# Performance work log

Hardware: AMD Instinct MI355X
Metric: run time of the kernel (lower is better)

The kernel has to match this reference:

```python
import jax, jax.numpy as jnp
import numpy as np

ALPHA_LINK = 2.0   # init arg alpha_link
TOP_K = 4096       # init arg top_k
BATCH = 65536
NUM_CLASSES = 4096


def setup_inputs() -> dict:
    key = jax.random.key(0)
    k1, k2, k3 = jax.random.split(key, 3)
    y_pred = jax.random.normal(k1, (BATCH, NUM_CLASSES), dtype=jnp.float32)
    y_true = jax.random.randint(k2, (BATCH,), 0, NUM_CLASSES, dtype=jnp.int32)
    # dense boolean link table: link_table[gt, pred] == True iff pred in link[gt]
    link_table = jax.random.randint(k3, (NUM_CLASSES, NUM_CLASSES), 0, 2, dtype=jnp.int32).astype(bool)
    return {"y_pred": y_pred, "y_true": y_true, "link_table": link_table}


def reference(y_pred, y_true, link_table):
    # vectorized replacement of the per-sample dict-lookup loop
    pred = jnp.argmax(y_pred, axis=1)                     # [B]
    linked = link_table[y_true, pred]                     # [B] bool
    # factor = alpha_link iff pred != gt and pred in link[gt]; else 1
    factor = jnp.where((pred != y_true) & linked, ALPHA_LINK, 1.0)
    # cross_entropy(reduction='none'), weight=None
    logp = jax.nn.log_softmax(y_pred, axis=1)             # [B, C]
    ce = -jnp.take_along_axis(logp, y_true[:, None], axis=1)[:, 0]  # [B]
    worst_k, _ = jax.lax.top_k(factor * ce, TOP_K)        # [TOP_K]
    return jnp.mean(worst_k)
```

## Files before the change

kernel.cpp:

```cpp
#include <hip/hip_runtime.h>

#define NCLS   4096
#define BATCHN 65536
#define TOPK   4096
#define ALPHA  2.0f

__global__ void detect_int32_kernel(const unsigned int* __restrict__ lt,
                                    int* __restrict__ flag) {
    int tid = threadIdx.x;
    unsigned int bad = 0;
    for (int i = tid; i < 1024; i += 64) bad |= (lt[i] > 1u) ? 1u : 0u;
    unsigned long long mask = __ballot(bad != 0);
    if (tid == 0) flag[0] = (mask == 0ULL) ? 1 : 0;
}

__device__ inline void amax_comb(float& m, int& mi, float om, int omi) {
    if (om > m || (om == m && omi < mi)) { m = om; mi = omi; }
}

__global__ __launch_bounds__(256) void row_loss_kernel(
    const float* __restrict__ yp, const int* __restrict__ yt,
    const unsigned char* __restrict__ lt, const int* __restrict__ flag,
    float* __restrict__ losses) {
    const int b   = blockIdx.x;
    const int tid = threadIdx.x;
    const float4* row = reinterpret_cast<const float4*>(yp + (size_t)b * NCLS);

    float4 v0 = row[0 * 256 + tid];
    float4 v1 = row[1 * 256 + tid];
    float4 v2 = row[2 * 256 + tid];
    float4 v3 = row[3 * 256 + tid];

    float m = -3.4e38f; int mi = 0;
    {
        const int c0 = tid * 4;
        if (v0.x > m) { m = v0.x; mi = c0 + 0; }
        if (v0.y > m) { m = v0.y; mi = c0 + 1; }
        if (v0.z > m) { m = v0.z; mi = c0 + 2; }
        if (v0.w > m) { m = v0.w; mi = c0 + 3; }
        const int c1 = 1024 + tid * 4;
        if (v1.x > m) { m = v1.x; mi = c1 + 0; }
        if (v1.y > m) { m = v1.y; mi = c1 + 1; }
        if (v1.z > m) { m = v1.z; mi = c1 + 2; }
        if (v1.w > m) { m = v1.w; mi = c1 + 3; }
        const int c2 = 2048 + tid * 4;
        if (v2.x > m) { m = v2.x; mi = c2 + 0; }
        if (v2.y > m) { m = v2.y; mi = c2 + 1; }
        if (v2.z > m) { m = v2.z; mi = c2 + 2; }
        if (v2.w > m) { m = v2.w; mi = c2 + 3; }
        const int c3 = 3072 + tid * 4;
        if (v3.x > m) { m = v3.x; mi = c3 + 0; }
        if (v3.y > m) { m = v3.y; mi = c3 + 1; }
        if (v3.z > m) { m = v3.z; mi = c3 + 2; }
        if (v3.w > m) { m = v3.w; mi = c3 + 3; }
    }

    #pragma unroll
    for (int off = 32; off > 0; off >>= 1) {
        float om  = __shfl_down(m, off, 64);
        int   omi = __shfl_down(mi, off, 64);
        amax_comb(m, mi, om, omi);
    }

    __shared__ float wmax[4];
    __shared__ int   wmi[4];
    __shared__ float wsum[4];
    __shared__ float s_M;
    __shared__ int   s_pred;
    __shared__ float s_true;

    const int wid = tid >> 6, lane = tid & 63;
    if (lane == 0) { wmax[wid] = m; wmi[wid] = mi; }
    __syncthreads();
    if (tid == 0) {
        float M = wmax[0]; int P = wmi[0];
        amax_comb(M, P, wmax[1], wmi[1]);
        amax_comb(M, P, wmax[2], wmi[2]);
        amax_comb(M, P, wmax[3], wmi[3]);
        s_M = M; s_pred = P;
    }
    __syncthreads();
    const float M = s_M;

    float sum = 0.f;
    sum += __expf(v0.x - M); sum += __expf(v0.y - M);
    sum += __expf(v0.z - M); sum += __expf(v0.w - M);
    sum += __expf(v1.x - M); sum += __expf(v1.y - M);
    sum += __expf(v1.z - M); sum += __expf(v1.w - M);
    sum += __expf(v2.x - M); sum += __expf(v2.y - M);
    sum += __expf(v2.z - M); sum += __expf(v2.w - M);
    sum += __expf(v3.x - M); sum += __expf(v3.y - M);
    sum += __expf(v3.z - M); sum += __expf(v3.w - M);

    #pragma unroll
    for (int off = 32; off > 0; off >>= 1) sum += __shfl_down(sum, off, 64);

    const int gt = yt[b];
    if (tid == ((gt >> 2) & 255)) {
        const int j = gt >> 10, k = gt & 3;
        float4 vv = (j == 0) ? v0 : (j == 1) ? v1 : (j == 2) ? v2 : v3;
        float t = (k == 0) ? vv.x : (k == 1) ? vv.y : (k == 2) ? vv.z : vv.w;
        s_true = t;
    }
    if (lane == 0) wsum[wid] = sum;
    __syncthreads();

    if (tid == 0) {
        float tot = wsum[0] + wsum[1] + wsum[2] + wsum[3];
        float ce  = logf(tot) + s_M - s_true;
        int pred  = s_pred;
        float factor = 1.0f;
        if (pred != gt) {
            size_t idx = (size_t)gt * NCLS + (size_t)pred;
            int linked = flag[0] ? ((const int*)lt)[idx] : (int)lt[idx];
            if (linked) factor = ALPHA;
        }
        losses[b] = factor * ce;
    }
}

__device__ void find_thresh_4096(unsigned int* hist, unsigned int* superb,
                                 int* s_t, unsigned int* s_above,
                                 unsigned int kneed, int tid) {
    if (tid < 64) {
        unsigned int s = 0;
        #pragma unroll 8
        for (int i = 0; i < 64; ++i) s += hist[tid * 64 + i];
        superb[tid] = s;
    }
    __syncthreads();
    if (tid == 0) {
        unsigned int cum = 0; int sb = 63;
        for (; sb > 0; --sb) {
            if (cum + superb[sb] >= kneed) break;
            cum += superb[sb];
        }
        const int lo = sb * 64;
        int t = lo + 63;
        for (; t > lo; --t) {
            if (cum + hist[t] >= kneed) break;
            cum += hist[t];
        }
        *s_t = t; *s_above = cum;
    }
    __syncthreads();
}

__global__ __launch_bounds__(1024) void topk_mean_kernel(
    const float* __restrict__ losses, float* __restrict__ out) {
    __shared__ unsigned int hist[4096];
    __shared__ unsigned int superb[64];
    __shared__ int          s_t;
    __shared__ unsigned int s_above;
    __shared__ unsigned int s_cntgt;
    __shared__ double       dsum[1024];

    const int tid = threadIdx.x;
    const int N = BATCHN, K = TOPK;
    unsigned int kneed = K;

    for (int i = tid; i < 4096; i += 1024) hist[i] = 0;
    __syncthreads();
    for (int i = tid; i < N; i += 1024) {
        unsigned int key = __float_as_uint(losses[i]);
        atomicAdd(&hist[key >> 20], 1u);
    }
    __syncthreads();
    find_thresh_4096(hist, superb, &s_t, &s_above, kneed, tid);
    const unsigned int t1 = (unsigned int)s_t;
    kneed -= s_above;
    __syncthreads();

    for (int i = tid; i < 4096; i += 1024) hist[i] = 0;
    __syncthreads();
    for (int i = tid; i < N; i += 1024) {
        unsigned int key = __float_as_uint(losses[i]);
        if ((key >> 20) == t1) atomicAdd(&hist[(key >> 8) & 0xFFFu], 1u);
    }
    __syncthreads();
    find_thresh_4096(hist, superb, &s_t, &s_above, kneed, tid);
    const unsigned int t2 = (unsigned int)s_t;
    kneed -= s_above;
    __syncthreads();

    const unsigned int pref = (t1 << 12) | t2;
    for (int i = tid; i < 256; i += 1024) hist[i] = 0;
    __syncthreads();
    for (int i = tid; i < N; i += 1024) {
        unsigned int key = __float_as_uint(losses[i]);
        if ((key >> 8) == pref) atomicAdd(&hist[key & 0xFFu], 1u);
    }
    __syncthreads();
    if (tid == 0) {
        unsigned int cum = 0; int t = 255;
        for (; t > 0; --t) {
            if (cum + hist[t] >= kneed) break;
            cum += hist[t];
        }
        s_t = t; s_above = cum;
    }
    __syncthreads();
    const unsigned int t3 = (unsigned int)s_t;
    const unsigned int T  = (pref << 8) | t3;

    double local = 0.0; unsigned int cgt = 0;
    for (int i = tid; i < N; i += 1024) {
        unsigned int key = __float_as_uint(losses[i]);
        if (key > T) { local += (double)__uint_as_float(key); cgt++; }
    }
    dsum[tid] = local;
    if (tid == 0) s_cntgt = 0;
    __syncthreads();
    atomicAdd(&s_cntgt, cgt);
    __syncthreads();
    for (int s = 512; s > 0; s >>= 1) {
        if (tid < s) dsum[tid] += dsum[tid + s];
        __syncthreads();
    }
    if (tid == 0) {
        unsigned int ngt = s_cntgt;
        double total = dsum[0] +
                       (double)(K - ngt) * (double)__uint_as_float(T);
        out[0] = (float)(total / (double)K);
    }
}

extern "C" void kernel_launch(void* const* d_in, const int* in_sizes, int n_in,
                              void* d_out, int out_size, void* d_ws, size_t ws_size,
                              hipStream_t stream) {
    const float* y_pred        = (const float*)d_in[0];
    const int* y_true          = (const int*)d_in[1];
    const unsigned char* lt    = (const unsigned char*)d_in[2];
    float* out                 = (float*)d_out;

    int*   flag   = (int*)d_ws;
    float* losses = (float*)((char*)d_ws + 1024);

    detect_int32_kernel<<<1, 64, 0, stream>>>((const unsigned int*)lt, flag);
    row_loss_kernel<<<BATCHN, 256, 0, stream>>>(y_pred, y_true, lt, flag, losses);
    topk_mean_kernel<<<1, 1024, 0, stream>>>(losses, out);
}
```

Measured before the change: 247.6 us.

## Persistent row-loss grid with row prefetch and fused first-level histogram

The row-loss kernel becomes a persistent grid of 2048 blocks that loops over rows and prefetches the next row into registers while it computes the current one. The argmax is split into a plain max reduction followed by a min-index search, and each row's loss is added with a global atomic to the first-pass histogram, so the top-k kernel skips one full pass over the losses. The top-k kernel replaces serial threshold scans with wave-level prefix sums and ballots and shrinks its final reduction. The costs are global atomics on a shared histogram, an extra memset launch, and higher register pressure from prefetching.

```diff
diff --git a/kernel.cpp b/kernel.cpp
--- a/kernel.cpp
+++ b/kernel.cpp
@@ -4,6 +4,7 @@
 #define BATCHN 65536
 #define TOPK   4096
 #define ALPHA  2.0f
+#define GRID_RL 2048
 
 __global__ void detect_int32_kernel(const unsigned int* __restrict__ lt,
                                     int* __restrict__ flag) {
@@ -14,229 +15,238 @@
     if (tid == 0) flag[0] = (mask == 0ULL) ? 1 : 0;
 }
 
-__device__ inline void amax_comb(float& m, int& mi, float om, int omi) {
-    if (om > m || (om == m && omi < mi)) { m = om; mi = omi; }
-}
-
 __global__ __launch_bounds__(256) void row_loss_kernel(
     const float* __restrict__ yp, const int* __restrict__ yt,
     const unsigned char* __restrict__ lt, const int* __restrict__ flag,
-    float* __restrict__ losses) {
-    const int b   = blockIdx.x;
+    float* __restrict__ losses, unsigned int* __restrict__ hist) {
+    const int tid  = threadIdx.x;
+    const int wid  = tid >> 6, lane = tid & 63;
+
+    __shared__ float wmax[4];
+    __shared__ float wsum[4];
+    __shared__ int   widx[4];
+    __shared__ float s_true;
+
+    int b = blockIdx.x;
+    {
+        const float4* rp = reinterpret_cast<const float4*>(yp + (size_t)b * NCLS);
+        float4 c0 = rp[tid], c1 = rp[256 + tid], c2 = rp[512 + tid], c3 = rp[768 + tid];
+
+        while (b < BATCHN) {
+            const int nb = b + GRID_RL;
+            float4 n0, n1, n2, n3;
+            if (nb < BATCHN) {
+                const float4* np_ = reinterpret_cast<const float4*>(yp + (size_t)nb * NCLS);
+                n0 = np_[tid]; n1 = np_[256 + tid]; n2 = np_[512 + tid]; n3 = np_[768 + tid];
+            }
+
+            float m = fmaxf(fmaxf(fmaxf(c0.x, c0.y), fmaxf(c0.z, c0.w)),
+                            fmaxf(fmaxf(c1.x, c1.y), fmaxf(c1.z, c1.w)));
+            m = fmaxf(m, fmaxf(fmaxf(fmaxf(c2.x, c2.y), fmaxf(c2.z, c2.w)),
+                               fmaxf(fmaxf(c3.x, c3.y), fmaxf(c3.z, c3.w))));
+            #pragma unroll
+            for (int off = 32; off > 0; off >>= 1)
+                m = fmaxf(m, __shfl_xor(m, off, 64));
+            if (lane == 0) wmax[wid] = m;
+
+            const int gt = yt[b];
+            if (tid == ((gt >> 2) & 255)) {
+                const int j = gt >> 10, k = gt & 3;
+                float4 vv = (j == 0) ? c0 : (j == 1) ? c1 : (j == 2) ? c2 : c3;
+                s_true = (k == 0) ? vv.x : (k == 1) ? vv.y : (k == 2) ? vv.z : vv.w;
+            }
+            __syncthreads();
+            const float M = fmaxf(fmaxf(wmax[0], wmax[1]), fmaxf(wmax[2], wmax[3]));
+
+            const int base = tid * 4;
+            int idx = 0x7fffffff;
+            if (c3.w == M) idx = 3072 + base + 3;
+            if (c3.z == M) idx = 3072 + base + 2;
+            if (c3.y == M) idx = 3072 + base + 1;
+            if (c3.x == M) idx = 3072 + base + 0;
+            if (c2.w == M) idx = 2048 + base + 3;
+            if (c2.z == M) idx = 2048 + base + 2;
+            if (c2.y == M) idx = 2048 + base + 1;
+            if (c2.x == M) idx = 2048 + base + 0;
+            if (c1.w == M) idx = 1024 + base + 3;
+            if (c1.z == M) idx = 1024 + base + 2;
+            if (c1.y == M) idx = 1024 + base + 1;
+            if (c1.x == M) idx = 1024 + base + 0;
+            if (c0.w == M) idx = base + 3;
+            if (c0.z == M) idx = base + 2;
+            if (c0.y == M) idx = base + 1;
+            if (c0.x == M) idx = base + 0;
+
+            float sum = 0.f;
+            sum += __expf(c0.x - M); sum += __expf(c0.y - M);
+            sum += __expf(c0.z - M); sum += __expf(c0.w - M);
+            sum += __expf(c1.x - M); sum += __expf(c1.y - M);
+            sum += __expf(c1.z - M); sum += __expf(c1.w - M);
+            sum += __expf(c2.x - M); sum += __expf(c2.y - M);
+            sum += __expf(c2.z - M); sum += __expf(c2.w - M);
+            sum += __expf(c3.x - M); sum += __expf(c3.y - M);
+            sum += __expf(c3.z - M); sum += __expf(c3.w - M);
+
+            #pragma unroll
+            for (int off = 32; off > 0; off >>= 1) {
+                sum += __shfl_xor(sum, off, 64);
+                idx  = min(idx, __shfl_xor(idx, off, 64));
+            }
+            if (lane == 0) { wsum[wid] = sum; widx[wid] = idx; }
+            __syncthreads();
+
+            if (tid == 0) {
+                const float tot = wsum[0] + wsum[1] + wsum[2] + wsum[3];
+                const int pred  = min(min(widx[0], widx[1]), min(widx[2], widx[3]));
+                const float ce  = logf(tot) + M - s_true;
+                float factor = 1.0f;
+                if (pred != gt) {
+                    const size_t li = (size_t)gt * NCLS + (size_t)pred;
+                    const int linked = flag[0] ? ((const int*)lt)[li] : (int)lt[li];
+                    if (linked) factor = ALPHA;
+                }
+                const float lv = factor * ce;
+                losses[b] = lv;
+                atomicAdd(&hist[__float_as_uint(lv) >> 20], 1u);
+            }
+            __syncthreads();
+
+            b = nb;
+            c0 = n0; c1 = n1; c2 = n2; c3 = n3;
+        }
+    }
+}
+
+__device__ inline void scan4096(const unsigned int* hist, unsigned int kneed,
+                                int* s_bin, unsigned int* s_kneed, int tid) {
+    if (tid < 64) {
+        unsigned int sb = 0;
+        #pragma unroll 8
+        for (int i = 0; i < 64; ++i) sb += hist[tid * 64 + i];
+        unsigned int GS = sb;
+        #pragma unroll
+        for (int off = 1; off < 64; off <<= 1) {
+            unsigned int o = __shfl_down(GS, off, 64);
+            GS += (tid + off < 64) ? o : 0u;
+        }
+        unsigned long long b1 = __ballot(GS >= kneed);
+        const int sstar = 63 - __clzll(b1);
+        const unsigned int A1 = (sstar < 63) ? __shfl(GS, sstar + 1, 64) : 0u;
+
+        unsigned int W = hist[sstar * 64 + tid];
+        #pragma unroll
+        for (int off = 1; off < 64; off <<= 1) {
+            unsigned int o = __shfl_down(W, off, 64);
+            W += (tid + off < 64) ? o : 0u;
+        }
+        unsigned long long b2 = __ballot(A1 + W >= kneed);
+        const int tstar = 63 - __clzll(b2);
+        const unsigned int above = A1 + ((tstar < 63) ? __shfl(W, tstar + 1, 64) : 0u);
+        if (tid == 0) { *s_bin = sstar * 64 + tstar; *s_kneed = kneed - above; }
+    }
+}
+
+__global__ __launch_bounds__(1024) void topk_mean_kernel(
+    const float* __restrict__ losses, const unsigned int* __restrict__ ghist,
+    float* __restrict__ out) {
+    __shared__ unsigned int hist[4096];
+    __shared__ int          s_bin;
+    __shared__ unsigned int s_kneed;
+    __shared__ double       dsum[16];
+    __shared__ unsigned int dcnt[16];
+
     const int tid = threadIdx.x;
-    const float4* row = reinterpret_cast<const float4*>(yp + (size_t)b * NCLS);
-
-    float4 v0 = row[0 * 256 + tid];
-    float4 v1 = row[1 * 256 + tid];
-    float4 v2 = row[2 * 256 + tid];
-    float4 v3 = row[3 * 256 + tid];
-
-    float m = -3.4e38f; int mi = 0;
-    {
-        const int c0 = tid * 4;
-        if (v0.x > m) { m = v0.x; mi = c0 + 0; }
-        if (v0.y > m) { m = v0.y; mi = c0 + 1; }
-        if (v0.z > m) { m = v0.z; mi = c0 + 2; }
-        if (v0.w > m) { m = v0.w; mi = c0 + 3; }
-        const int c1 = 1024 + tid * 4;
-        if (v1.x > m) { m = v1.x; mi = c1 + 0; }
-        if (v1.y > m) { m = v1.y; mi = c1 + 1; }
-        if (v1.z > m) { m = v1.z; mi = c1 + 2; }
-        if (v1.w > m) { m = v1.w; mi = c1 + 3; }
-        const int c2 = 2048 + tid * 4;
-        if (v2.x > m) { m = v2.x; mi = c2 + 0; }
-        if (v2.y > m) { m = v2.y; mi = c2 + 1; }
-        if (v2.z > m) { m = v2.z; mi = c2 + 2; }
-        if (v2.w > m) { m = v2.w; mi = c2 + 3; }
-        const int c3 = 3072 + tid * 4;
-        if (v3.x > m) { m = v3.x; mi = c3 + 0; }
-        if (v3.y > m) { m = v3.y; mi = c3 + 1; }
-        if (v3.z > m) { m = v3.z; mi = c3 + 2; }
-        if (v3.w > m) { m = v3.w; mi = c3 + 3; }
-    }
-
+    const int N = BATCHN, K = TOPK;
+
+    for (int i = tid; i < 4096; i += 1024) hist[i] = ghist[i];
+    __syncthreads();
+    scan4096(hist, (unsigned int)K, &s_bin, &s_kneed, tid);
+    __syncthreads();
+    const unsigned int t1 = (unsigned int)s_bin;
+    const unsigned int k1 = s_kneed;
+    __syncthreads();
+
+    for (int i = tid; i < 4096; i += 1024) hist[i] = 0;
+    __syncthreads();
+    for (int i = tid; i < N; i += 1024) {
+        const unsigned int key = __float_as_uint(losses[i]);
+        if ((key >> 20) == t1) atomicAdd(&hist[(key >> 8) & 0xFFFu], 1u);
+    }
+    __syncthreads();
+    scan4096(hist, k1, &s_bin, &s_kneed, tid);
+    __syncthreads();
+    const unsigned int t2 = (unsigned int)s_bin;
+    const unsigned int k2 = s_kneed;
+    const unsigned int pref = (t1 << 12) | t2;
+    __syncthreads();
+
+    for (int i = tid; i < 256; i += 1024) hist[i] = 0;
+    __syncthreads();
+    for (int i = tid; i < N; i += 1024) {
+        const unsigned int key = __float_as_uint(losses[i]);
+        if ((key >> 8) == pref) atomicAdd(&hist[key & 0xFFu], 1u);
+    }
+    __syncthreads();
+    if (tid < 64) {
+        unsigned int sb = hist[tid * 4] + hist[tid * 4 + 1] +
+                          hist[tid * 4 + 2] + hist[tid * 4 + 3];
+        unsigned int GS = sb;
+        #pragma unroll
+        for (int off = 1; off < 64; off <<= 1) {
+            unsigned int o = __shfl_down(GS, off, 64);
+            GS += (tid + off < 64) ? o : 0u;
+        }
+        unsigned long long b1 = __ballot(GS >= k2);
+        const int sstar = 63 - __clzll(b1);
+        const unsigned int A1 = (sstar < 63) ? __shfl(GS, sstar + 1, 64) : 0u;
+        if (tid == 0) {
+            unsigned int G = A1; int tstar = sstar * 4; unsigned int above = A1;
+            for (int j = 3; j >= 0; --j) {
+                const int bin = sstar * 4 + j;
+                if (G + hist[bin] >= k2) { tstar = bin; above = G; break; }
+                G += hist[bin];
+            }
+            s_bin = tstar; s_kneed = k2 - above; (void)s_kneed;
+        }
+    }
+    __syncthreads();
+    const unsigned int T = (pref << 8) | (unsigned int)s_bin;
+
+    double local = 0.0; unsigned int cgt = 0;
+    for (int i = tid; i < N; i += 1024) {
+        const unsigned int key = __float_as_uint(losses[i]);
+        if (key > T) { local += (double)__uint_as_float(key); cgt++; }
+    }
+    const int wid = tid >> 6, lane = tid & 63;
     #pragma unroll
     for (int off = 32; off > 0; off >>= 1) {
-        float om  = __shfl_down(m, off, 64);
-        int   omi = __shfl_down(mi, off, 64);
-        amax_comb(m, mi, om, omi);
-    }
-
-    __shared__ float wmax[4];
-    __shared__ int   wmi[4];
-    __shared__ float wsum[4];
-    __shared__ float s_M;
-    __shared__ int   s_pred;
-    __shared__ float s_true;
-
-    const int wid = tid >> 6, lane = tid & 63;
-    if (lane == 0) { wmax[wid] = m; wmi[wid] = mi; }
+        local += __shfl_down(local, off, 64);
+        cgt   += __shfl_down(cgt, off, 64);
+    }
+    if (lane == 0) { dsum[wid] = local; dcnt[wid] = cgt; }
     __syncthreads();
     if (tid == 0) {
-        float M = wmax[0]; int P = wmi[0];
-        amax_comb(M, P, wmax[1], wmi[1]);
-        amax_comb(M, P, wmax[2], wmi[2]);
-        amax_comb(M, P, wmax[3], wmi[3]);
-        s_M = M; s_pred = P;
-    }
-    __syncthreads();
-    const float M = s_M;
-
-    float sum = 0.f;
-    sum += __expf(v0.x - M); sum += __expf(v0.y - M);
-    sum += __expf(v0.z - M); sum += __expf(v0.w - M);
-    sum += __expf(v1.x - M); sum += __expf(v1.y - M);
-    sum += __expf(v1.z - M); sum += __expf(v1.w - M);
-    sum += __expf(v2.x - M); sum += __expf(v2.y - M);
-    sum += __expf(v2.z - M); sum += __expf(v2.w - M);
-    sum += __expf(v3.x - M); sum += __expf(v3.y - M);
-    sum += __expf(v3.z - M); sum += __expf(v3.w - M);
-
-    #pragma unroll
-    for (int off = 32; off > 0; off >>= 1) sum += __shfl_down(sum, off, 64);
-
-    const int gt = yt[b];
-    if (tid == ((gt >> 2) & 255)) {
-        const int j = gt >> 10, k = gt & 3;
-        float4 vv = (j == 0) ? v0 : (j == 1) ? v1 : (j == 2) ? v2 : v3;
-        float t = (k == 0) ? vv.x : (k == 1) ? vv.y : (k == 2) ? vv.z : vv.w;
-        s_true = t;
-    }
-    if (lane == 0) wsum[wid] = sum;
-    __syncthreads();
-
-    if (tid == 0) {
-        float tot = wsum[0] + wsum[1] + wsum[2] + wsum[3];
-        float ce  = logf(tot) + s_M - s_true;
-        int pred  = s_pred;
-        float factor = 1.0f;
-        if (pred != gt) {
-            size_t idx = (size_t)gt * NCLS + (size_t)pred;
-            int linked = flag[0] ? ((const int*)lt)[idx] : (int)lt[idx];
-            if (linked) factor = ALPHA;
-        }
-        losses[b] = factor * ce;
-    }
-}
-
-__device__ void find_thresh_4096(unsigned int* hist, unsigned int* superb,
-                                 int* s_t, unsigned int* s_above,
-                                 unsigned int kneed, int tid) {
-    if (tid < 64) {
-        unsigned int s = 0;
-        #pragma unroll 8
-        for (int i = 0; i < 64; ++i) s += hist[tid * 64 + i];
-        superb[tid] = s;
-    }
-    __syncthreads();
-    if (tid == 0) {
-        unsigned int cum = 0; int sb = 63;
-        for (; sb > 0; --sb) {
-            if (cum + superb[sb] >= kneed) break;
-            cum += superb[sb];
-        }
-        const int lo = sb * 64;
-        int t = lo + 63;
-        for (; t > lo; --t) {
-            if (cum + hist[t] >= kneed) break;
-            cum += hist[t];
-        }
-        *s_t = t; *s_above = cum;
-    }
-    __syncthreads();
-}
-
-__global__ __launch_bounds__(1024) void topk_mean_kernel(
-    const float* __restrict__ losses, float* __restrict__ out) {
-    __shared__ unsigned int hist[4096];
-    __shared__ unsigned int superb[64];
-    __shared__ int          s_t;
-    __shared__ unsigned int s_above;
-    __shared__ unsigned int s_cntgt;
-    __shared__ double       dsum[1024];
-
-    const int tid = threadIdx.x;
-    const int N = BATCHN, K = TOPK;
-    unsigned int kneed = K;
-
-    for (int i = tid; i < 4096; i += 1024) hist[i] = 0;
-    __syncthreads();
-    for (int i = tid; i < N; i += 1024) {
-        unsigned int key = __float_as_uint(losses[i]);
-        atomicAdd(&hist[key >> 20], 1u);
-    }
-    __syncthreads();
-    find_thresh_4096(hist, superb, &s_t, &s_above, kneed, tid);
-    const unsigned int t1 = (unsigned int)s_t;
-    kneed -= s_above;
-    __syncthreads();
-
-    for (int i = tid; i < 4096; i += 1024) hist[i] = 0;
-    __syncthreads();
-    for (int i = tid; i < N; i += 1024) {
-        unsigned int key = __float_as_uint(losses[i]);
-        if ((key >> 20) == t1) atomicAdd(&hist[(key >> 8) & 0xFFFu], 1u);
-    }
-    __syncthreads();
-    find_thresh_4096(hist, superb, &s_t, &s_above, kneed, tid);
-    const unsigned int t2 = (unsigned int)s_t;
-    kneed -= s_above;
-    __syncthreads();
-
-    const unsigned int pref = (t1 << 12) | t2;
-    for (int i = tid; i < 256; i += 1024) hist[i] = 0;
-    __syncthreads();
-    for (int i = tid; i < N; i += 1024) {
-        unsigned int key = __float_as_uint(losses[i]);
-        if ((key >> 8) == pref) atomicAdd(&hist[key & 0xFFu], 1u);
-    }
-    __syncthreads();
-    if (tid == 0) {
-        unsigned int cum = 0; int t = 255;
-        for (; t > 0; --t) {
-            if (cum + hist[t] >= kneed) break;
-            cum += hist[t];
-        }
-        s_t = t; s_above = cum;
-    }
-    __syncthreads();
-    const unsigned int t3 = (unsigned int)s_t;
-    const unsigned int T  = (pref << 8) | t3;
-
-    double local = 0.0; unsigned int cgt = 0;
-    for (int i = tid; i < N; i += 1024) {
-        unsigned int key = __float_as_uint(losses[i]);
-        if (key > T) { local += (double)__uint_as_float(key); cgt++; }
-    }
-    dsum[tid] = local;
-    if (tid == 0) s_cntgt = 0;
-    __syncthreads();
-    atomicAdd(&s_cntgt, cgt);
-    __syncthreads();
-    for (int s = 512; s > 0; s >>= 1) {
-        if (tid < s) dsum[tid] += dsum[tid + s];
-        __syncthreads();
-    }
-    if (tid == 0) {
-        unsigned int ngt = s_cntgt;
-        double total = dsum[0] +
-                       (double)(K - ngt) * (double)__uint_as_float(T);
-        out[0] = (float)(total / (double)K);
+        double tot = 0.0; unsigned int ngt = 0;
+        for (int w = 0; w < 16; ++w) { tot += dsum[w]; ngt += dcnt[w]; }
+        tot += (double)(K - ngt) * (double)__uint_as_float(T);
+        out[0] = (float)(tot / (double)K);
     }
 }
 
 extern "C" void kernel_launch(void* const* d_in, const int* in_sizes, int n_in,
                               void* d_out, int out_size, void* d_ws, size_t ws_size,
                               hipStream_t stream) {
-    const float* y_pred        = (const float*)d_in[0];
-    const int* y_true          = (const int*)d_in[1];
-    const unsigned char* lt    = (const unsigned char*)d_in[2];
-    float* out                 = (float*)d_out;
-
-    int*   flag   = (int*)d_ws;
-    float* losses = (float*)((char*)d_ws + 1024);
+    const float* y_pred     = (const float*)d_in[0];
+    const int* y_true       = (const int*)d_in[1];
+    const unsigned char* lt = (const unsigned char*)d_in[2];
+    float* out              = (float*)d_out;
+
+    int*          flag   = (int*)d_ws;
+    unsigned int* hist   = (unsigned int*)((char*)d_ws + 1024);
+    float*        losses = (float*)((char*)d_ws + 32768);
 
     detect_int32_kernel<<<1, 64, 0, stream>>>((const unsigned int*)lt, flag);
-    row_loss_kernel<<<BATCHN, 256, 0, stream>>>(y_pred, y_true, lt, flag, losses);
-    topk_mean_kernel<<<1, 1024, 0, stream>>>(losses, out);
-}
+    hipMemsetAsync(hist, 0, 4096 * sizeof(unsigned int), stream);
+    row_loss_kernel<<<GRID_RL, 256, 0, stream>>>(y_pred, y_true, lt, flag, losses, hist);
+    topk_mean_kernel<<<1, 1024, 0, stream>>>(losses, hist, out);
+}
```

Measured after the change: 793.9 us. +220.6%, slower.
